# Optimization experiments

Hardware: AMD Instinct MI355X
Metric: run time of the kernel (lower is better)

Reference implementation:

```python
import jax, jax.numpy as jnp
import numpy as np

B, T, C, H, DH = 2, 2048, 768, 12, 64


def setup_inputs() -> dict:
    key = jax.random.key(0)
    k1, k2, k3 = jax.random.split(key, 3)
    x = jax.random.normal(k1, (B, T, C), dtype=jnp.float32)
    Wqkv = jax.random.normal(k2, (C, 3 * C), dtype=jnp.float32) * (C ** -0.5)
    Wout = jax.random.normal(k3, (C, C), dtype=jnp.float32) * (C ** -0.5)
    return {"x": x, "Wqkv": Wqkv, "Wout": Wout}


def reference(x, Wqkv, Wout):
    b, t, c = x.shape
    qkv = x @ Wqkv  # [B,T,3C]
    q, k, v = jnp.split(qkv, 3, axis=-1)
    # [B,T,C] -> [B,H,T,dh]
    q = q.reshape(b, t, H, DH).transpose(0, 2, 1, 3)
    k = k.reshape(b, t, H, DH).transpose(0, 2, 1, 3)
    v = v.reshape(b, t, H, DH).transpose(0, 2, 1, 3)
    scale = DH ** -0.5
    scores = jnp.einsum('bhqd,bhkd->bhqk', q, k) * scale  # [B,H,T,T]
    causal = jnp.tril(jnp.ones((t, t), dtype=bool))
    scores = jnp.where(causal, scores, -jnp.inf)
    weights = jax.nn.softmax(scores, axis=-1)
    # dropout p=0.0 -> identity
    out = jnp.einsum('bhqk,bhkd->bhqd', weights, v)  # [B,H,T,dh]
    out = out.transpose(0, 2, 1, 3).reshape(b, t, c)
    return out @ Wout
```

## Files before the change

kernel.cpp:

```cpp
#include <hip/hip_runtime.h>
#include <hip/hip_bf16.h>

#define Bn 2
#define Tn 2048
#define Cn 768
#define Hn 12
#define Dn 64
#define N3n 2304
#define Mn 4096

#define MASKVAL (-30000.f)
#define NITEMS 768
#define DEFER_THR 64.f

typedef unsigned short u16;
typedef __attribute__((ext_vector_type(8))) unsigned short ushort8_t;
typedef __attribute__((ext_vector_type(8))) short bf16x8;
typedef __attribute__((ext_vector_type(4))) float f32x4;

__device__ __forceinline__ float bf2f(u16 u) {
  union { unsigned int i; float f; } v; v.i = ((unsigned int)u) << 16; return v.f;
}
__device__ __forceinline__ u16 f2bf(float f) {
  union { float f; unsigned int i; } v; v.f = f;
  return (u16)((v.i + 0x7fffu + ((v.i >> 16) & 1u)) >> 16);
}
__device__ __forceinline__ float safe_exp(float x) {
  return __expf(fmaxf(x, -80.f));
}

__global__ __launch_bounds__(256) void cast_bf16(const float* __restrict__ in,
                                                 u16* __restrict__ out,
                                                 int* __restrict__ counter) {
  if (blockIdx.x == 0 && threadIdx.x == 0) *counter = 0;
  const int i = (blockIdx.x * 256 + threadIdx.x) * 4;
  float4 v = *(const float4*)(in + i);
  ushort4 s;
  s.x = f2bf(v.x); s.y = f2bf(v.y); s.z = f2bf(v.z); s.w = f2bf(v.w);
  *(ushort4*)(out + i) = s;
}

__global__ __launch_bounds__(256) void transpose_cast(const float* __restrict__ in,
                                                      u16* __restrict__ out,
                                                      int R, int Cc) {
  __shared__ u16 t[32][33];
  const int c0 = blockIdx.x * 32, r0 = blockIdx.y * 32;
  const int tx = threadIdx.x, ty = threadIdx.y;
#pragma unroll
  for (int i = 0; i < 4; i++)
    t[ty * 4 + i][tx] = f2bf(in[(size_t)(r0 + ty * 4 + i) * Cc + c0 + tx]);
  __syncthreads();
#pragma unroll
  for (int i = 0; i < 4; i++)
    out[(size_t)(c0 + ty * 4 + i) * R + r0 + tx] = t[tx][ty * 4 + i];
}

#define GP 40

template <int EPI>
__global__ __launch_bounds__(256) void mfma_gemm(const u16* __restrict__ A,
                                                 const u16* __restrict__ BT,
                                                 u16* __restrict__ Q,
                                                 u16* __restrict__ Kd,
                                                 u16* __restrict__ VT,
                                                 float* __restrict__ out) {
  __shared__ __align__(16) u16 Ash[128 * GP];
  __shared__ __align__(16) u16 Bsh[128 * GP];
  const int tid = threadIdx.x;
  const int wv = tid >> 6, lane = tid & 63;
  const int lo = lane & 15, quad = lane >> 4;
  const int wm = wv & 1, wn = wv >> 1;
  const int n0 = blockIdx.x * 128;
  const int m0 = blockIdx.y * 128;

  f32x4 acc[4][4];
#pragma unroll
  for (int i = 0; i < 4; i++)
#pragma unroll
    for (int j = 0; j < 4; j++) acc[i][j] = f32x4{0.f, 0.f, 0.f, 0.f};

  for (int k0 = 0; k0 < Cn; k0 += 32) {
    __syncthreads();
#pragma unroll
    for (int it = 0; it < 2; it++) {
      const int c = tid + it * 256;
      const int row = c >> 2, col = (c & 3) << 3;
      *(ushort8_t*)&Ash[row * GP + col] =
          *(const ushort8_t*)(A + (size_t)(m0 + row) * Cn + k0 + col);
      *(ushort8_t*)&Bsh[row * GP + col] =
          *(const ushort8_t*)(BT + (size_t)(n0 + row) * Cn + k0 + col);
    }
    __syncthreads();

    bf16x8 af[4], bfr[4];
#pragma unroll
    for (int t = 0; t < 4; t++) {
      af[t]  = *(const bf16x8*)&Ash[(wm * 64 + t * 16 + lo) * GP + (quad << 3)];
      bfr[t] = *(const bf16x8*)&Bsh[(wn * 64 + t * 16 + lo) * GP + (quad << 3)];
    }
#pragma unroll
    for (int mt = 0; mt < 4; mt++)
#pragma unroll
      for (int nt = 0; nt < 4; nt++)
        acc[mt][nt] = __builtin_amdgcn_mfma_f32_16x16x32_bf16(af[mt], bfr[nt],
                                                              acc[mt][nt], 0, 0, 0);
  }

  if (EPI == 0) {
    const int which = n0 / Cn;
    const int h = ((n0 % Cn) >> 6) + wn;
    const int bb = m0 >> 11;
    const int t_base = (m0 & (Tn - 1)) + wm * 64;
    if (which < 2) {
      u16* dst = ((which == 0) ? Q : Kd) + (size_t)(bb * Hn + h) * Tn * Dn;
#pragma unroll
      for (int mt = 0; mt < 4; mt++)
#pragma unroll
        for (int nt = 0; nt < 4; nt++)
#pragma unroll
          for (int r = 0; r < 4; r++) {
            const int t = t_base + mt * 16 + (quad << 2) + r;
            dst[(size_t)t * Dn + nt * 16 + lo] = f2bf(acc[mt][nt][r]);
          }
    } else {
      u16* dst = VT + (size_t)(bb * Hn + h) * Dn * Tn;
#pragma unroll
      for (int mt = 0; mt < 4; mt++)
#pragma unroll
        for (int nt = 0; nt < 4; nt++) {
          const int t = t_base + mt * 16 + (quad << 2);
          const int d = nt * 16 + lo;
          ushort4 st;
          st.x = f2bf(acc[mt][nt][0]); st.y = f2bf(acc[mt][nt][1]);
          st.z = f2bf(acc[mt][nt][2]); st.w = f2bf(acc[mt][nt][3]);
          *(ushort4*)&dst[(size_t)d * Tn + t] = st;
        }
    }
  } else {
#pragma unroll
    for (int mt = 0; mt < 4; mt++)
#pragma unroll
      for (int nt = 0; nt < 4; nt++)
#pragma unroll
        for (int r = 0; r < 4; r++) {
          const int m = m0 + wm * 64 + mt * 16 + (quad << 2) + r;
          out[(size_t)m * Cn + n0 + wn * 64 + nt * 16 + lo] = acc[mt][nt][r];
        }
  }
}

#define KP 72
#define TILE_W (64 * KP)

__global__ __launch_bounds__(256) void attn_kernel(const u16* __restrict__ Q,
                                                   const u16* __restrict__ K,
                                                   const u16* __restrict__ VT,
                                                   u16* __restrict__ O,
                                                   int* __restrict__ counter) {
  __shared__ __align__(16) u16 Ksh[2 * TILE_W];
  __shared__ __align__(16) u16 Vsh[2 * TILE_W];
  __shared__ __align__(16) u16 Pw[4][16 * KP];
  __shared__ int s_item;

  const int tid = threadIdx.x;
  const int wv = tid >> 6, lane = tid & 63;
  const int lo = lane & 15, quad = lane >> 4;
  const int sr = tid >> 3;
  const int sc = (tid & 7) << 3;

  for (;;) {
    if (tid == 0) s_item = atomicAdd(counter, 1);
    __syncthreads();
    const int item = s_item;
    if (item >= NITEMS) return;

    const int q0 = (31 - item / 24) * 64;
    const int hb = item % 24;
    const int h = hb % 12, b = hb / 12;
    const size_t base = (size_t)(b * Hn + h) * Tn * Dn;
    const size_t vtb  = (size_t)(b * Hn + h) * Dn * Tn;

    const u16* qp = Q + base + (size_t)(q0 + (wv << 4) + lo) * Dn + (quad << 3);
    const bf16x8 aq0 = *(const bf16x8*)qp;
    const bf16x8 aq1 = *(const bf16x8*)(qp + 32);

    f32x4 o[4] = {f32x4{0,0,0,0}, f32x4{0,0,0,0}, f32x4{0,0,0,0}, f32x4{0,0,0,0}};
    float m1 = MASKVAL;
    float l1 = 0.f;

#pragma unroll
    for (int it = 0; it < 2; it++) {
      const int r = sr + it * 32;
      *(ushort8_t*)&Ksh[r * KP + sc] =
          *(const ushort8_t*)(K + base + (size_t)r * Dn + sc);
      *(ushort8_t*)&Vsh[r * KP + sc] =
          *(const ushort8_t*)(VT + vtb + (size_t)r * Tn + sc);
    }
    __syncthreads();

    int cur = 0;
    const int qrel = (wv << 4) + lo;

    for (int j0 = 0; j0 <= q0; j0 += 64) {
      const bool hasnext = (j0 + 64 <= q0);

      ushort8_t kr[2], vr[2];
      if (hasnext) {
#pragma unroll
        for (int it = 0; it < 2; it++) {
          const int r = sr + it * 32;
          kr[it] = *(const ushort8_t*)(K + base + (size_t)(j0 + 64 + r) * Dn + sc);
          vr[it] = *(const ushort8_t*)(VT + vtb + (size_t)r * Tn + j0 + 64 + sc);
        }
      }

      const u16* Kb_ = &Ksh[cur * TILE_W];
      const u16* Vb_ = &Vsh[cur * TILE_W];

      f32x4 s[4];
#pragma unroll
      for (int nt = 0; nt < 4; nt++) {
        const bf16x8 bk0 = *(const bf16x8*)(&Kb_[(nt * 16 + lo) * KP + (quad << 3)]);
        const bf16x8 bk1 = *(const bf16x8*)(&Kb_[(nt * 16 + lo) * KP + 32 + (quad << 3)]);
        f32x4 a = {0.f, 0.f, 0.f, 0.f};
        a = __builtin_amdgcn_mfma_f32_16x16x32_bf16(bk0, aq0, a, 0, 0, 0);
        a = __builtin_amdgcn_mfma_f32_16x16x32_bf16(bk1, aq1, a, 0, 0, 0);
        s[nt] = a;
      }

      if (j0 == q0) {
#pragma unroll
        for (int nt = 0; nt < 4; nt++)
#pragma unroll
          for (int r = 0; r < 4; r++) {
            const int kv = nt * 16 + (quad << 2) + r;
            if (kv > qrel) s[nt][r] = MASKVAL;
          }
      }

      const float mxa = fmaxf(fmaxf(s[0][0], s[0][1]), fmaxf(s[0][2], s[0][3]));
      const float mxb = fmaxf(fmaxf(s[1][0], s[1][1]), fmaxf(s[1][2], s[1][3]));
      const float mxc = fmaxf(fmaxf(s[2][0], s[2][1]), fmaxf(s[2][2], s[2][3]));
      const float mxd = fmaxf(fmaxf(s[3][0], s[3][1]), fmaxf(s[3][2], s[3][3]));
      const float pmax = fmaxf(fmaxf(mxa, mxb), fmaxf(mxc, mxd));

      if (!__all(pmax <= m1 + DEFER_THR)) {
        float mx = pmax;
        mx = fmaxf(mx, __shfl_xor(mx, 16));
        mx = fmaxf(mx, __shfl_xor(mx, 32));
        const float mnew = fmaxf(m1, mx);
        const float alpha = safe_exp(0.125f * (m1 - mnew));
        m1 = mnew;
        l1 *= alpha;
        float ar[4];
#pragma unroll
        for (int r = 0; r < 4; r++) ar[r] = __shfl(alpha, (quad << 2) + r);
#pragma unroll
        for (int nt = 0; nt < 4; nt++)
#pragma unroll
          for (int r = 0; r < 4; r++) o[nt][r] *= ar[r];
      }

      const float mb = 0.125f * m1;
      float sum = 0.f;
#pragma unroll
      for (int nt = 0; nt < 4; nt++)
#pragma unroll
        for (int r = 0; r < 4; r++) {
          const float p = safe_exp(0.125f * s[nt][r] - mb);
          s[nt][r] = p;
          sum += p;
        }
      l1 += sum;

      u16* pw = Pw[wv];
#pragma unroll
      for (int nt = 0; nt < 4; nt++) {
        ushort4 pk;
        pk.x = f2bf(s[nt][0]); pk.y = f2bf(s[nt][1]);
        pk.z = f2bf(s[nt][2]); pk.w = f2bf(s[nt][3]);
        *(ushort4*)&pw[lo * KP + nt * 16 + (quad << 2)] = pk;
      }
      const bf16x8 pa0 = *(const bf16x8*)(&pw[lo * KP + (quad << 3)]);
      const bf16x8 pa1 = *(const bf16x8*)(&pw[lo * KP + 32 + (quad << 3)]);

#pragma unroll
      for (int nt = 0; nt < 4; nt++) {
        const bf16x8 bv0 = *(const bf16x8*)(&Vb_[(nt * 16 + lo) * KP + (quad << 3)]);
        const bf16x8 bv1 = *(const bf16x8*)(&Vb_[(nt * 16 + lo) * KP + 32 + (quad << 3)]);
        o[nt] = __builtin_amdgcn_mfma_f32_16x16x32_bf16(pa0, bv0, o[nt], 0, 0, 0);
        o[nt] = __builtin_amdgcn_mfma_f32_16x16x32_bf16(pa1, bv1, o[nt], 0, 0, 0);
      }

      if (hasnext) {
        const int nb = cur ^ 1;
#pragma unroll
        for (int it = 0; it < 2; it++) {
          const int r = sr + it * 32;
          *(ushort8_t*)&Ksh[nb * TILE_W + r * KP + sc] = kr[it];
          *(ushort8_t*)&Vsh[nb * TILE_W + r * KP + sc] = vr[it];
        }
      }
      __syncthreads();
      cur ^= 1;
    }

    float lt = l1;
    lt += __shfl_xor(lt, 16);
    lt += __shfl_xor(lt, 32);
    const float linv = 1.f / lt;
    float ir[4];
#pragma unroll
    for (int r = 0; r < 4; r++) ir[r] = __shfl(linv, (quad << 2) + r);
#pragma unroll
    for (int nt = 0; nt < 4; nt++)
#pragma unroll
      for (int r = 0; r < 4; r++) {
        const int row = q0 + (wv << 4) + (quad << 2) + r;
        const int col = h * 64 + nt * 16 + lo;
        O[(size_t)(b * Tn + row) * Cn + col] = f2bf(o[nt][r] * ir[r]);
      }
  }
}

extern "C" void kernel_launch(void* const* d_in, const int* in_sizes, int n_in,
                              void* d_out, int out_size, void* d_ws, size_t ws_size,
                              hipStream_t stream) {
  const float* x    = (const float*)d_in[0];
  const float* Wqkv = (const float*)d_in[1];
  const float* Wout = (const float*)d_in[2];
  float* out = (float*)d_out;

  const size_t per = (size_t)Bn * Hn * Tn * Dn;
  u16* xb    = (u16*)d_ws;
  u16* WqkvT = xb + (size_t)Mn * Cn;
  u16* WoutT = WqkvT + (size_t)N3n * Cn;
  u16* Qb    = WoutT + (size_t)Cn * Cn;
  u16* Kb    = Qb + per;
  u16* VTb   = Kb + per;
  u16* attn  = VTb + per;
  int* counter = (int*)(attn + (size_t)Mn * Cn);

  cast_bf16<<<(Mn * Cn) / 1024, 256, 0, stream>>>(x, xb, counter);
  transpose_cast<<<dim3(N3n / 32, Cn / 32), dim3(32, 8), 0, stream>>>(Wqkv, WqkvT, Cn, N3n);
  transpose_cast<<<dim3(Cn / 32, Cn / 32), dim3(32, 8), 0, stream>>>(Wout, WoutT, Cn, Cn);

  mfma_gemm<0><<<dim3(N3n / 128, Mn / 128), 256, 0, stream>>>(xb, WqkvT, Qb, Kb, VTb, nullptr);
  attn_kernel<<<dim3(512), 256, 0, stream>>>(Qb, Kb, VTb, attn, counter);
  mfma_gemm<1><<<dim3(Cn / 128, Mn / 128), 256, 0, stream>>>(attn, WoutT, nullptr, nullptr, nullptr, out);
}
```

Baseline: 186.0 us.

## Use direct global-to-LDS loads, XCD swizzle, exp2 softmax and packed bf16 conversion

The GEMM now uses a 64-wide K tile filled by global_load_lds direct-to-LDS loads, and remaps workgroup IDs so neighbouring tiles land on the same XCD for L2 reuse. The attention kernel raises wave priority around the MFMA blocks and replaces the clamped __expf with exp2f on prescaled scores. It also packs probabilities with v_cvt_pk_bf16_f32 and launches more persistent blocks. Together these aim to cut load instruction overhead and softmax ALU cost. The unpadded LDS layout may cause bank conflicts, and dropping the exp clamp changes how underflow is handled.

```diff
diff --git a/kernel.cpp b/kernel.cpp
--- a/kernel.cpp
+++ b/kernel.cpp
@@ -12,11 +12,14 @@
 #define MASKVAL (-30000.f)
 #define NITEMS 768
 #define DEFER_THR 64.f
+#define L2E8 0.1803368801111204f
 
 typedef unsigned short u16;
 typedef __attribute__((ext_vector_type(8))) unsigned short ushort8_t;
 typedef __attribute__((ext_vector_type(8))) short bf16x8;
 typedef __attribute__((ext_vector_type(4))) float f32x4;
+typedef __attribute__((address_space(1))) unsigned int* gas1_t;
+typedef __attribute__((address_space(3))) unsigned int* las3_t;
 
 __device__ __forceinline__ float bf2f(u16 u) {
   union { unsigned int i; float f; } v; v.i = ((unsigned int)u) << 16; return v.f;
@@ -24,9 +27,6 @@
 __device__ __forceinline__ u16 f2bf(float f) {
   union { float f; unsigned int i; } v; v.f = f;
   return (u16)((v.i + 0x7fffu + ((v.i >> 16) & 1u)) >> 16);
-}
-__device__ __forceinline__ float safe_exp(float x) {
-  return __expf(fmaxf(x, -80.f));
 }
 
 __global__ __launch_bounds__(256) void cast_bf16(const float* __restrict__ in,
@@ -55,7 +55,7 @@
     out[(size_t)(c0 + ty * 4 + i) * R + r0 + tx] = t[tx][ty * 4 + i];
 }
 
-#define GP 40
+#define BK 64
 
 template <int EPI>
 __global__ __launch_bounds__(256) void mfma_gemm(const u16* __restrict__ A,
@@ -64,14 +64,22 @@
                                                  u16* __restrict__ Kd,
                                                  u16* __restrict__ VT,
                                                  float* __restrict__ out) {
-  __shared__ __align__(16) u16 Ash[128 * GP];
-  __shared__ __align__(16) u16 Bsh[128 * GP];
+  __shared__ __align__(16) u16 Ash[128 * BK];
+  __shared__ __align__(16) u16 Bsh[128 * BK];
   const int tid = threadIdx.x;
   const int wv = tid >> 6, lane = tid & 63;
   const int lo = lane & 15, quad = lane >> 4;
   const int wm = wv & 1, wn = wv >> 1;
-  const int n0 = blockIdx.x * 128;
-  const int m0 = blockIdx.y * 128;
+
+  const int nwg = gridDim.x * gridDim.y;
+  const int cpx = nwg >> 3;
+  const int lid = blockIdx.y * gridDim.x + blockIdx.x;
+  const int swz = (lid & 7) * cpx + (lid >> 3);
+  const int n0 = (swz % gridDim.x) * 128;
+  const int m0 = (swz / gridDim.x) * 128;
+
+  const int srow = lane >> 3;
+  const int scol = (lane & 7) << 3;
 
   f32x4 acc[4][4];
 #pragma unroll
@@ -79,31 +87,39 @@
 #pragma unroll
     for (int j = 0; j < 4; j++) acc[i][j] = f32x4{0.f, 0.f, 0.f, 0.f};
 
-  for (int k0 = 0; k0 < Cn; k0 += 32) {
+  for (int k0 = 0; k0 < Cn; k0 += BK) {
     __syncthreads();
 #pragma unroll
-    for (int it = 0; it < 2; it++) {
-      const int c = tid + it * 256;
-      const int row = c >> 2, col = (c & 3) << 3;
-      *(ushort8_t*)&Ash[row * GP + col] =
-          *(const ushort8_t*)(A + (size_t)(m0 + row) * Cn + k0 + col);
-      *(ushort8_t*)&Bsh[row * GP + col] =
-          *(const ushort8_t*)(BT + (size_t)(n0 + row) * Cn + k0 + col);
+    for (int c = 0; c < 4; c++) {
+      const int rb = (wv << 5) + (c << 3);
+      const int gr = rb + srow;
+      __builtin_amdgcn_global_load_lds(
+          (gas1_t)(A + (size_t)(m0 + gr) * Cn + k0 + scol),
+          (las3_t)(&Ash[rb * BK]), 16, 0, 0);
+      __builtin_amdgcn_global_load_lds(
+          (gas1_t)(BT + (size_t)(n0 + gr) * Cn + k0 + scol),
+          (las3_t)(&Bsh[rb * BK]), 16, 0, 0);
     }
     __syncthreads();
 
-    bf16x8 af[4], bfr[4];
+    bf16x8 af[4][2], bfr[4][2];
 #pragma unroll
     for (int t = 0; t < 4; t++) {
-      af[t]  = *(const bf16x8*)&Ash[(wm * 64 + t * 16 + lo) * GP + (quad << 3)];
-      bfr[t] = *(const bf16x8*)&Bsh[(wn * 64 + t * 16 + lo) * GP + (quad << 3)];
+#pragma unroll
+      for (int s = 0; s < 2; s++) {
+        af[t][s]  = *(const bf16x8*)&Ash[(wm * 64 + t * 16 + lo) * BK + s * 32 + (quad << 3)];
+        bfr[t][s] = *(const bf16x8*)&Bsh[(wn * 64 + t * 16 + lo) * BK + s * 32 + (quad << 3)];
+      }
     }
 #pragma unroll
     for (int mt = 0; mt < 4; mt++)
 #pragma unroll
-      for (int nt = 0; nt < 4; nt++)
-        acc[mt][nt] = __builtin_amdgcn_mfma_f32_16x16x32_bf16(af[mt], bfr[nt],
+      for (int nt = 0; nt < 4; nt++) {
+        acc[mt][nt] = __builtin_amdgcn_mfma_f32_16x16x32_bf16(af[mt][0], bfr[nt][0],
                                                               acc[mt][nt], 0, 0, 0);
+        acc[mt][nt] = __builtin_amdgcn_mfma_f32_16x16x32_bf16(af[mt][1], bfr[nt][1],
+                                                              acc[mt][nt], 0, 0, 0);
+      }
   }
 
   if (EPI == 0) {
@@ -218,6 +234,7 @@
       const u16* Vb_ = &Vsh[cur * TILE_W];
 
       f32x4 s[4];
+      __builtin_amdgcn_s_setprio(1);
 #pragma unroll
       for (int nt = 0; nt < 4; nt++) {
         const bf16x8 bk0 = *(const bf16x8*)(&Kb_[(nt * 16 + lo) * KP + (quad << 3)]);
@@ -227,6 +244,7 @@
         a = __builtin_amdgcn_mfma_f32_16x16x32_bf16(bk1, aq1, a, 0, 0, 0);
         s[nt] = a;
       }
+      __builtin_amdgcn_s_setprio(0);
 
       if (j0 == q0) {
 #pragma unroll
@@ -238,18 +256,21 @@
           }
       }
 
-      const float mxa = fmaxf(fmaxf(s[0][0], s[0][1]), fmaxf(s[0][2], s[0][3]));
-      const float mxb = fmaxf(fmaxf(s[1][0], s[1][1]), fmaxf(s[1][2], s[1][3]));
-      const float mxc = fmaxf(fmaxf(s[2][0], s[2][1]), fmaxf(s[2][2], s[2][3]));
-      const float mxd = fmaxf(fmaxf(s[3][0], s[3][1]), fmaxf(s[3][2], s[3][3]));
-      const float pmax = fmaxf(fmaxf(mxa, mxb), fmaxf(mxc, mxd));
+      float mx = fmaxf(s[0][0], s[0][1]);
+      mx = fmaxf(fmaxf(mx, s[0][2]), s[0][3]);
+      mx = fmaxf(fmaxf(mx, s[1][0]), s[1][1]);
+      mx = fmaxf(fmaxf(mx, s[1][2]), s[1][3]);
+      mx = fmaxf(fmaxf(mx, s[2][0]), s[2][1]);
+      mx = fmaxf(fmaxf(mx, s[2][2]), s[2][3]);
+      mx = fmaxf(fmaxf(mx, s[3][0]), s[3][1]);
+      mx = fmaxf(fmaxf(mx, s[3][2]), s[3][3]);
+      const float pmax = mx;
 
       if (!__all(pmax <= m1 + DEFER_THR)) {
-        float mx = pmax;
-        mx = fmaxf(mx, __shfl_xor(mx, 16));
-        mx = fmaxf(mx, __shfl_xor(mx, 32));
-        const float mnew = fmaxf(m1, mx);
-        const float alpha = safe_exp(0.125f * (m1 - mnew));
+        float mr = fmaxf(pmax, __shfl_xor(pmax, 16));
+        mr = fmaxf(mr, __shfl_xor(mr, 32));
+        const float mnew = fmaxf(m1, mr);
+        const float alpha = __builtin_amdgcn_exp2f(L2E8 * (m1 - mnew));
         m1 = mnew;
         l1 *= alpha;
         float ar[4];
@@ -261,13 +282,13 @@
           for (int r = 0; r < 4; r++) o[nt][r] *= ar[r];
       }
 
-      const float mb = 0.125f * m1;
+      const float mb2 = L2E8 * m1;
       float sum = 0.f;
 #pragma unroll
       for (int nt = 0; nt < 4; nt++)
 #pragma unroll
         for (int r = 0; r < 4; r++) {
-          const float p = safe_exp(0.125f * s[nt][r] - mb);
+          const float p = __builtin_amdgcn_exp2f(L2E8 * s[nt][r] - mb2);
           s[nt][r] = p;
           sum += p;
         }
@@ -276,14 +297,15 @@
       u16* pw = Pw[wv];
 #pragma unroll
       for (int nt = 0; nt < 4; nt++) {
-        ushort4 pk;
-        pk.x = f2bf(s[nt][0]); pk.y = f2bf(s[nt][1]);
-        pk.z = f2bf(s[nt][2]); pk.w = f2bf(s[nt][3]);
-        *(ushort4*)&pw[lo * KP + nt * 16 + (quad << 2)] = pk;
+        unsigned int p01, p23;
+        asm("v_cvt_pk_bf16_f32 %0, %1, %2" : "=v"(p01) : "v"(s[nt][0]), "v"(s[nt][1]));
+        asm("v_cvt_pk_bf16_f32 %0, %1, %2" : "=v"(p23) : "v"(s[nt][2]), "v"(s[nt][3]));
+        *(uint2*)&pw[lo * KP + nt * 16 + (quad << 2)] = make_uint2(p01, p23);
       }
       const bf16x8 pa0 = *(const bf16x8*)(&pw[lo * KP + (quad << 3)]);
       const bf16x8 pa1 = *(const bf16x8*)(&pw[lo * KP + 32 + (quad << 3)]);
 
+      __builtin_amdgcn_s_setprio(1);
 #pragma unroll
       for (int nt = 0; nt < 4; nt++) {
         const bf16x8 bv0 = *(const bf16x8*)(&Vb_[(nt * 16 + lo) * KP + (quad << 3)]);
@@ -291,6 +313,7 @@
         o[nt] = __builtin_amdgcn_mfma_f32_16x16x32_bf16(pa0, bv0, o[nt], 0, 0, 0);
         o[nt] = __builtin_amdgcn_mfma_f32_16x16x32_bf16(pa1, bv1, o[nt], 0, 0, 0);
       }
+      __builtin_amdgcn_s_setprio(0);
 
       if (hasnext) {
         const int nb = cur ^ 1;
@@ -346,6 +369,6 @@
   transpose_cast<<<dim3(Cn / 32, Cn / 32), dim3(32, 8), 0, stream>>>(Wout, WoutT, Cn, Cn);
 
   mfma_gemm<0><<<dim3(N3n / 128, Mn / 128), 256, 0, stream>>>(xb, WqkvT, Qb, Kb, VTb, nullptr);
-  attn_kernel<<<dim3(512), 256, 0, stream>>>(Qb, Kb, VTb, attn, counter);
+  attn_kernel<<<dim3(640), 256, 0, stream>>>(Qb, Kb, VTb, attn, counter);
   mfma_gemm<1><<<dim3(Cn / 128, Mn / 128), 256, 0, stream>>>(attn, WoutT, nullptr, nullptr, nullptr, out);
 }
```

After: 181.2 us. 1.03x faster.
